# Performance work log

Hardware: AMD Instinct MI355X
Metric: run time of the kernel (lower is better)

## Reference

```python
import jax, jax.numpy as jnp
import numpy as np

B, L, H = 2, 4096, 1024


def _rope_tables(seq_len, dim, base=10000.0):
    # standard RoPE cos/sin tables, rotate-half convention, shape [L, dim]
    inv_freq = 1.0 / (base ** (np.arange(0, dim, 2, dtype=np.float32) / dim))
    t = np.arange(seq_len, dtype=np.float32)
    freqs = np.outer(t, inv_freq)                      # [L, dim/2]
    emb = np.concatenate([freqs, freqs], axis=-1)      # [L, dim]
    return jnp.asarray(np.cos(emb)), jnp.asarray(np.sin(emb))


def setup_inputs() -> dict:
    key = jax.random.key(0)
    k1, k2 = jax.random.split(key)
    hidden_states = jax.random.normal(k1, (B, L, H), dtype=jnp.float32)
    # queries weight: normal with std = initializer_range / sqrt(2*num_layers*hidden)
    std = 0.02 / np.sqrt(2.0 * 24 * H)
    W_q = jax.random.normal(k2, (H, H), dtype=jnp.float32) * std
    cos, sin = _rope_tables(L, H)
    return {"hidden_states": hidden_states, "W_q": W_q, "cos": cos, "sin": sin}


def _rotate_half(x):
    x1, x2 = jnp.split(x, 2, axis=-1)
    return jnp.concatenate([-x2, x1], axis=-1)


def reference(hidden_states, W_q, cos, sin):
    # dropout with p=0.0 (eval) -> identity
    h = hidden_states * cos[None, :, :] + _rotate_half(hidden_states) * sin[None, :, :]  # RoPE, [B,L,H]
    q = jnp.einsum('blh,oh->blo', h, W_q)          # F.linear(h, W_q), [B,L,H]
    pre_attn = jnp.einsum('blh,bmh->blm', q, h)    # Q @ K^T (no softmax), [B,L,L]
    attention = jnp.einsum('blm,bmh->blh', pre_attn, h)  # scores @ V, [B,L,H]
    return attention
```

## Files before the change

### kernel.cpp

```cpp
#include <hip/hip_runtime.h>
#include <hip/hip_bf16.h>
#include <stdint.h>

#define BB 2
#define LL 4096
#define HH 1024
#define GBK 32

typedef __bf16 bf16;
typedef __bf16 bf16x4 __attribute__((ext_vector_type(4)));
typedef __bf16 bf16x8 __attribute__((ext_vector_type(8)));
typedef float  f32x4  __attribute__((ext_vector_type(4)));

__device__ __forceinline__ void async_cp16(const bf16* g, const bf16* l)
{
    typedef const uint32_t __attribute__((address_space(1)))* gp_t;
    typedef uint32_t __attribute__((address_space(3)))* lp_t;
    __builtin_amdgcn_global_load_lds((gp_t)(uintptr_t)g, (lp_t)(uintptr_t)l, 16, 0, 0);
}

__global__ __launch_bounds__(128) void rope_kernel(
    const float* __restrict__ x, const float* __restrict__ cs,
    const float* __restrict__ sn, bf16* __restrict__ h)
{
    const int l = blockIdx.x;
    const int b = blockIdx.y;
    const int i = threadIdx.x * 4;
    const long xb = ((long)b * LL + l) * HH;
    const long cb = (long)l * HH;

    const float4 x1 = *(const float4*)(x + xb + i);
    const float4 x2 = *(const float4*)(x + xb + i + HH / 2);
    const float4 c1 = *(const float4*)(cs + cb + i);
    const float4 c2 = *(const float4*)(cs + cb + i + HH / 2);
    const float4 s1 = *(const float4*)(sn + cb + i);
    const float4 s2 = *(const float4*)(sn + cb + i + HH / 2);

    bf16x4 o1, o2;
    o1[0] = (bf16)(x1.x * c1.x - x2.x * s1.x);
    o1[1] = (bf16)(x1.y * c1.y - x2.y * s1.y);
    o1[2] = (bf16)(x1.z * c1.z - x2.z * s1.z);
    o1[3] = (bf16)(x1.w * c1.w - x2.w * s1.w);
    o2[0] = (bf16)(x2.x * c2.x + x1.x * s2.x);
    o2[1] = (bf16)(x2.y * c2.y + x1.y * s2.y);
    o2[2] = (bf16)(x2.z * c2.z + x1.z * s2.z);
    o2[3] = (bf16)(x2.w * c2.w + x1.w * s2.w);

    *(bf16x4*)(h + xb + i)          = o1;
    *(bf16x4*)(h + xb + i + HH / 2) = o2;
}

__global__ __launch_bounds__(256) void transpose_bf16_64(
    const bf16* __restrict__ in, bf16* __restrict__ out, const int R, const int C)
{
    __shared__ uint32_t lds[64][36];
    const long zoff = (long)blockIdx.z * R * C;
    const int r0 = blockIdx.x * 64;
    const int c0 = blockIdx.y * 64;
    const int t  = threadIdx.x;

    const int c8 = t & 7;
    const int rr = t >> 3;
    const bf16* p0 = in + zoff + (long)(r0 + 2 * rr) * C + c0 + c8 * 8;
    const uint4 ra = *(const uint4*)p0;
    const uint4 rb = *(const uint4*)(p0 + C);
    const uint32_t av[4] = {ra.x, ra.y, ra.z, ra.w};
    const uint32_t bv[4] = {rb.x, rb.y, rb.z, rb.w};
#pragma unroll
    for (int j = 0; j < 4; ++j) {
        const uint32_t alo = av[j] & 0xffffu, ahi = av[j] >> 16;
        const uint32_t blo = bv[j] & 0xffffu, bhi = bv[j] >> 16;
        lds[c8 * 8 + 2 * j    ][rr] = alo | (blo << 16);
        lds[c8 * 8 + 2 * j + 1][rr] = ahi | (bhi << 16);
    }
    __syncthreads();

    const int c = t >> 2;
    const int q = t & 3;
    const uint4 w0 = *(const uint4*)&lds[c][q * 8];
    const uint4 w1 = *(const uint4*)&lds[c][q * 8 + 4];
    bf16* po = out + zoff + (long)(c0 + c) * R + r0 + q * 16;
    *(uint4*)(po)     = w0;
    *(uint4*)(po + 8) = w1;
}

__global__ __launch_bounds__(256) void cast_wq(
    const float* __restrict__ Wq, bf16* __restrict__ Wb)
{
    const long idx = ((long)blockIdx.x * 256 + threadIdx.x) * 4;
    const float4 v = *(const float4*)(Wq + idx);
    bf16x4 o;
    o[0] = (bf16)v.x; o[1] = (bf16)v.y; o[2] = (bf16)v.z; o[3] = (bf16)v.w;
    *(bf16x4*)(Wb + idx) = o;
}

#define GEMM_SHARED()                                                          \
    __shared__ __align__(16) bf16 As_[2][128][32];                             \
    __shared__ __align__(16) bf16 Bs_[2][128][32];

#define GEMM_PREFETCH(KOFF, BUF)                                               \
    do {                                                                       \
        async_cp16(Ag + (KOFF),           &As_[BUF][0][0] + woff0);            \
        async_cp16(Ag + (KOFF) + 64L * K, &As_[BUF][0][0] + woff1);            \
        async_cp16(Bg + (KOFF),           &Bs_[BUF][0][0] + woff0);            \
        async_cp16(Bg + (KOFF) + 64L * K, &Bs_[BUF][0][0] + woff1);            \
    } while (0)

#define GEMM_BODY(M0, N0, KBASE, KEND, DST, DT, LDN)                           \
    {                                                                          \
        const int tid  = threadIdx.x;                                          \
        const int lane = tid & 63;                                             \
        const int wave = tid >> 6;                                             \
        const int wm = (wave & 1) * 64;                                        \
        const int wn = (wave >> 1) * 64;                                       \
        const int fr = lane & 15;                                              \
        const int fq = lane >> 4;                                              \
        const int srow = tid >> 2;                                             \
        const int scol = (tid & 3) * 8;                                        \
        const int woff0 = wave * 512;                                          \
        const int woff1 = 2048 + wave * 512;                                   \
        const bf16* Ag = Ab + (long)((M0) + srow) * K + scol;                  \
        const bf16* Bg = Bb + (long)((N0) + srow) * K + scol;                  \
        const f32x4 vzero = {0.f, 0.f, 0.f, 0.f};                              \
        f32x4 acc[4][4];                                                       \
        _Pragma("unroll") for (int i = 0; i < 4; ++i)                          \
            _Pragma("unroll") for (int j = 0; j < 4; ++j) acc[i][j] = vzero;   \
        GEMM_PREFETCH(KBASE, 0);                                               \
        int buf = 0;                                                           \
        for (int k0 = (KBASE); k0 < (KEND); k0 += GBK, buf ^= 1) {             \
            __syncthreads();                                                   \
            if (k0 + GBK < (KEND)) GEMM_PREFETCH(k0 + GBK, buf ^ 1);           \
            bf16x8 af[4], bfv[4];                                              \
            _Pragma("unroll") for (int i = 0; i < 4; ++i)                      \
                af[i]  = *(const bf16x8*)&As_[buf][wm + i * 16 + fr][fq * 8];  \
            _Pragma("unroll") for (int j = 0; j < 4; ++j)                      \
                bfv[j] = *(const bf16x8*)&Bs_[buf][wn + j * 16 + fr][fq * 8];  \
            _Pragma("unroll") for (int i = 0; i < 4; ++i)                      \
                _Pragma("unroll") for (int j = 0; j < 4; ++j)                  \
                    acc[i][j] = __builtin_amdgcn_mfma_f32_16x16x32_bf16(       \
                        af[i], bfv[j], acc[i][j], 0, 0, 0);                    \
        }                                                                      \
        _Pragma("unroll") for (int i = 0; i < 4; ++i) {                        \
            _Pragma("unroll") for (int r = 0; r < 4; ++r) {                    \
                const int row = (M0) + wm + i * 16 + fq * 4 + r;               \
                _Pragma("unroll") for (int j = 0; j < 4; ++j) {                \
                    const int col = (N0) + wn + j * 16 + fr;                   \
                    (DST)[(long)row * (LDN) + col] = (DT)acc[i][j][r];         \
                }                                                              \
            }                                                                  \
        }                                                                      \
    }

template <typename OUT_T>
__global__ __launch_bounds__(256) void gemm_bt(
    const bf16* __restrict__ A, const bf16* __restrict__ B, OUT_T* __restrict__ C,
    const int M, const int N, const int K,
    const long sA, const long sB, const long sC)
{
    GEMM_SHARED();
    const bf16* Ab = A + blockIdx.z * sA;
    const bf16* Bb = B + blockIdx.z * sB;
    OUT_T*      Cb = C + blockIdx.z * sC;
    const int m0 = blockIdx.x * 128;
    const int n0 = blockIdx.y * 128;
    GEMM_BODY(m0, n0, 0, K, Cb, OUT_T, N);
}

#define E_STAGE_A(KT, PART, BUF)                                               \
  do {                                                                         \
    const int kk0_ = kbase + (KT) * 64;                                        \
    _Pragma("unroll") for (int qq_ = 0; qq_ < 2; ++qq_) {                      \
      const int ch_  = qq_ * 512 + tid;                                        \
      const int sl_  = ch_ >> 3;                                               \
      const int cc_  = (ch_ & 7) ^ (sl_ & 7);                                  \
      const int row_ = (sl_ & 63) + (PART) * 64 + ((sl_ >> 6) << 7);           \
      async_cp16(Ab + (long)(m0 + row_) * K + kk0_ + cc_ * 8,                  \
                 &As[BUF][PART][0][0] + (qq_ * 512 + (tid & 448)) * 8);        \
    }                                                                          \
  } while (0)

#define E_STAGE_B(KT, PART, BUF)                                               \
  do {                                                                         \
    const int kk0_ = kbase + (KT) * 64;                                        \
    _Pragma("unroll") for (int qq_ = 0; qq_ < 2; ++qq_) {                      \
      const int ch_  = qq_ * 512 + tid;                                        \
      const int sl_  = ch_ >> 3;                                               \
      const int cc_  = (ch_ & 7) ^ (sl_ & 7);                                  \
      const int row_ = (sl_ & 31) + (PART) * 32 + ((sl_ >> 5) << 6);           \
      async_cp16(Bb + (long)(n0 + row_) * K + kk0_ + cc_ * 8,                  \
                 &Bs[BUF][PART][0][0] + (qq_ * 512 + (tid & 448)) * 8);        \
    }                                                                          \
  } while (0)

#define E_LOAD_A(BUF, IG)                                                      \
  do {                                                                         \
    const bf16* Ap_ = &As[BUF][IG][0][0] + (wr * 64 + fr) * 64;                \
    _Pragma("unroll") for (int ii_ = 0; ii_ < 4; ++ii_)                        \
      _Pragma("unroll") for (int kk_ = 0; kk_ < 2; ++kk_)                      \
        af[ii_][kk_] = *(const bf16x8*)(Ap_ + ii_ * 1024 +                     \
                        (((kk_ * 4 + fq) ^ fr7) * 8));                         \
  } while (0)

#define E_LOAD_B(BUF, JP)                                                      \
  do {                                                                         \
    const bf16* Bp_ = &Bs[BUF][JP][0][0] + (wc * 32 + fr) * 64;                \
    _Pragma("unroll") for (int jj_ = 0; jj_ < 2; ++jj_)                        \
      _Pragma("unroll") for (int kk_ = 0; kk_ < 2; ++kk_)                      \
        bfv[jj_][kk_] = *(const bf16x8*)(Bp_ + jj_ * 1024 +                    \
                        (((kk_ * 4 + fq) ^ fr7) * 8));                         \
  } while (0)

#define E_MMA(IG, JG)                                                          \
  do {                                                                         \
    __builtin_amdgcn_s_setprio(1);                                             \
    _Pragma("unroll") for (int ii_ = 0; ii_ < 4; ++ii_)                        \
      _Pragma("unroll") for (int jj_ = 0; jj_ < 2; ++jj_)                      \
        _Pragma("unroll") for (int kk_ = 0; kk_ < 2; ++kk_)                    \
          acc[(IG) * 4 + ii_][(JG) * 2 + jj_] =                                \
              __builtin_amdgcn_mfma_f32_16x16x32_bf16(                         \
                  af[ii_][kk_], bfv[jj_][kk_],                                 \
                  acc[(IG) * 4 + ii_][(JG) * 2 + jj_], 0, 0, 0);               \
    __builtin_amdgcn_s_setprio(0);                                             \
  } while (0)

#define E_BAR()   __builtin_amdgcn_s_barrier()
#define E_LGKM0() do { asm volatile("s_waitcnt lgkmcnt(0)" ::: "memory");      \
                       __builtin_amdgcn_sched_barrier(0); } while (0)
#define E_VM(N)   asm volatile("s_waitcnt vmcnt(" #N ")" ::: "memory")

#define ENGINE_PREAMBLE()                                                      \
  __shared__ __align__(16) bf16 As[2][2][128][64];                             \
  __shared__ __align__(16) bf16 Bs[2][2][128][64];                             \
  const int tid  = threadIdx.x;                                                \
  const int lane = tid & 63;                                                   \
  const int wv   = tid >> 6;                                                   \
  const int wr   = wv >> 2;                                                    \
  const int wc   = wv & 3;                                                     \
  const int fr   = lane & 15;                                                  \
  const int fq   = lane >> 4;                                                  \
  const int fr7  = fr & 7;                                                     \
  bf16x8 af[4][2], bfv[2][2];                                                  \
  f32x4 acc[8][4];                                                             \
  _Pragma("unroll") for (int i_ = 0; i_ < 8; ++i_)                             \
    _Pragma("unroll") for (int j_ = 0; j_ < 4; ++j_)                           \
      acc[i_][j_] = (f32x4){0.f, 0.f, 0.f, 0.f};

#define ENGINE_LOOP(NT)                                                        \
    \
  E_STAGE_A(0, 0, 0); E_STAGE_B(0, 1, 0); E_STAGE_A(0, 1, 0);                  \
  E_STAGE_B(0, 0, 0);                                                          \
  E_STAGE_A(1, 0, 1); E_STAGE_B(1, 1, 1); E_STAGE_A(1, 1, 1);                  \
  E_VM(6); E_BAR();                                                            \
  int t_ = 0;                                                                  \
  _Pragma("unroll 1") for (; t_ + 3 < (NT); t_ += 2) {                         \
     E_LOAD_A(0, 0); E_LOAD_B(0, 0); E_STAGE_B(t_ + 1, 0, 1);          \
             E_BAR(); E_LGKM0(); E_MMA(0, 0); E_BAR();                         \
     E_LOAD_B(0, 1); E_STAGE_A(t_ + 2, 0, 0);                          \
             E_BAR(); E_LGKM0(); E_MMA(0, 1); E_BAR();                         \
     E_LOAD_A(0, 1); E_STAGE_B(t_ + 2, 1, 0);                          \
             E_BAR(); E_LGKM0(); E_MMA(1, 1); E_BAR();                         \
     E_LOAD_B(0, 0); E_STAGE_A(t_ + 2, 1, 0);                          \
             E_BAR(); E_LGKM0(); E_MMA(1, 0); E_VM(6); E_BAR();                \
     E_LOAD_A(1, 0); E_LOAD_B(1, 0); E_STAGE_B(t_ + 2, 0, 0);          \
             E_BAR(); E_LGKM0(); E_MMA(0, 0); E_BAR();                         \
     E_LOAD_B(1, 1); E_STAGE_A(t_ + 3, 0, 1);                          \
             E_BAR(); E_LGKM0(); E_MMA(0, 1); E_BAR();                         \
     E_LOAD_A(1, 1); E_STAGE_B(t_ + 3, 1, 1);                          \
             E_BAR(); E_LGKM0(); E_MMA(1, 1); E_BAR();                         \
     E_LOAD_B(1, 0); E_STAGE_A(t_ + 3, 1, 1);                          \
             E_BAR(); E_LGKM0(); E_MMA(1, 0); E_VM(6); E_BAR();                \
  }                                                                            \
                  \
  E_LOAD_A(0, 0); E_LOAD_B(0, 0); E_STAGE_B(t_ + 1, 0, 1);                     \
  E_BAR(); E_LGKM0(); E_MMA(0, 0); E_BAR();                                    \
  E_LOAD_B(0, 1); E_BAR(); E_LGKM0(); E_MMA(0, 1); E_BAR();                    \
  E_LOAD_A(0, 1); E_BAR(); E_LGKM0(); E_MMA(1, 1); E_BAR();                    \
  E_LOAD_B(0, 0); E_BAR(); E_LGKM0(); E_MMA(1, 0); E_VM(0); E_BAR();           \
  E_LOAD_A(1, 0); E_LOAD_B(1, 0); E_BAR(); E_LGKM0(); E_MMA(0, 0); E_BAR();    \
  E_LOAD_B(1, 1); E_BAR(); E_LGKM0(); E_MMA(0, 1); E_BAR();                    \
  E_LOAD_A(1, 1); E_BAR(); E_LGKM0(); E_MMA(1, 1); E_BAR();                    \
  E_LOAD_B(1, 0); E_BAR(); E_LGKM0(); E_MMA(1, 0);

#define ENGINE_STORE(DST, DT, LDN)                                             \
  _Pragma("unroll") for (int gi_ = 0; gi_ < 8; ++gi_) {                        \
    _Pragma("unroll") for (int r_ = 0; r_ < 4; ++r_) {                         \
      const int row_ = m0 + wr * 128 + gi_ * 16 + fq * 4 + r_;                 \
      _Pragma("unroll") for (int gj_ = 0; gj_ < 4; ++gj_) {                    \
        const int col_ = n0 + wc * 64 + gj_ * 16 + fr;                         \
        (DST)[(long)row_ * (LDN) + col_] = (DT)acc[gi_][gj_][r_];              \
      }                                                                        \
    }                                                                          \
  }

__global__ __launch_bounds__(512, 2) void gemm8_Gq(
    const bf16* __restrict__ hT, const bf16* __restrict__ Wb,
    const bf16* __restrict__ h, float* __restrict__ P, bf16* __restrict__ q)
{
    ENGINE_PREAMBLE();
    const int id = blockIdx.x;
    const bf16* Ab; const bf16* Bb;
    int K, kbase, m0, n0;
    float* Pc = nullptr;
    if (id < 128) {
        m0 = (id & 31) * 256;
        n0 = (id >> 5) * 256;
        Ab = h; Bb = Wb; K = HH; kbase = 0;
    } else {
        const int u  = id - 128;
        const int zb = u >> 6;
        const int v  = u & 63;
        const int zs = v >> 4;
        const int tl = v & 15;
        m0 = (tl & 3) * 256;
        n0 = (tl >> 2) * 256;
        Ab = hT + (long)zb * HH * LL; Bb = Ab;
        K  = LL; kbase = zs * (LL / 4);
        Pc = P + (long)(zb * 4 + zs) * HH * HH;
    }
    ENGINE_LOOP(16);
    if (Pc) { ENGINE_STORE(Pc, float, HH); }
    else    { ENGINE_STORE(q,  bf16,  HH); }
}

__global__ __launch_bounds__(512, 2) void gemm8_qG(
    const bf16* __restrict__ q, const bf16* __restrict__ G, float* __restrict__ out)
{
    ENGINE_PREAMBLE();
    const int id = blockIdx.x;
    const int b  = id >> 6;
    const int u  = id & 63;
    const int m0 = (u & 15) * 256;
    const int n0 = (u >> 4) * 256;
    const bf16* Ab = q + (long)b * LL * HH;
    const bf16* Bb = G + (long)b * HH * HH;
    const int K = HH, kbase = 0;
    float* outb = out + (long)b * LL * HH;
    ENGINE_LOOP(16);
    ENGINE_STORE(outb, float, HH);
}

__global__ __launch_bounds__(256) void reduce_splits(
    const float* __restrict__ P, bf16* __restrict__ out, const int npb, const int S)
{
    const int b = blockIdx.y;
    const long r = ((long)blockIdx.x * 256 + threadIdx.x) * 4;
    const float* base = P + (long)b * S * npb + r;
    float4 a = *(const float4*)(base);
    for (int s = 1; s < S; ++s) {
        const float4 v = *(const float4*)(base + (long)s * npb);
        a.x += v.x; a.y += v.y; a.z += v.z; a.w += v.w;
    }
    bf16x4 o;
    o[0] = (bf16)a.x; o[1] = (bf16)a.y; o[2] = (bf16)a.z; o[3] = (bf16)a.w;
    *(bf16x4*)(out + (long)b * npb + r) = o;
}

extern "C" void kernel_launch(void* const* d_in, const int* in_sizes, int n_in,
                              void* d_out, int out_size, void* d_ws, size_t ws_size,
                              hipStream_t stream)
{
    const float* x  = (const float*)d_in[0];
    const float* Wq = (const float*)d_in[1];
    const float* cs = (const float*)d_in[2];
    const float* sn = (const float*)d_in[3];
    float* out = (float*)d_out;
    char* ws = (char*)d_ws;

    bf16*  h  = (bf16*)(ws);
    bf16*  hT = (bf16*)(ws + 16u * 1024 * 1024);
    bf16*  Wb = (bf16*)(ws + 32u * 1024 * 1024);
    bf16*  G  = (bf16*)(ws + 34u * 1024 * 1024);
    float* P  = (float*)(ws + 38u * 1024 * 1024);

    const bool big_ws = ws_size >= (size_t)90 * 1024 * 1024;
    bf16* q = big_ws ? (bf16*)(ws + 70u * 1024 * 1024)
                     : (bf16*)(ws + 38u * 1024 * 1024);

    rope_kernel<<<dim3(LL, BB), 128, 0, stream>>>(x, cs, sn, h);

    transpose_bf16_64<<<dim3(LL / 64, HH / 64, BB), 256, 0, stream>>>(h, hT, LL, HH);

    cast_wq<<<dim3(HH * HH / 1024), 256, 0, stream>>>(Wq, Wb);

    if (big_ws) {
        gemm8_Gq<<<dim3(256), 512, 0, stream>>>(hT, Wb, h, P, q);
        reduce_splits<<<dim3(HH * HH / 1024, BB), 256, 0, stream>>>(P, G, HH * HH, 4);
        gemm8_qG<<<dim3(128), 512, 0, stream>>>(q, G, out);
    } else {
        gemm_bt<bf16><<<dim3(HH / 128, HH / 128, BB), 256, 0, stream>>>(
            hT, hT, G, HH, HH, LL, (long)HH * LL, (long)HH * LL, (long)HH * HH);
        gemm_bt<bf16><<<dim3(LL / 128, HH / 128, BB), 256, 0, stream>>>(
            h, Wb, q, LL, HH, HH, (long)LL * HH, 0L, (long)LL * HH);
        gemm_bt<float><<<dim3(LL / 128, HH / 128, BB), 256, 0, stream>>>(
            q, G, out, LL, HH, HH, (long)LL * HH, (long)HH * HH, (long)LL * HH);
    }
}
```

Before: 190.9 us.

## Fuse RoPE, transpose and weight cast; halve final GEMM tile for more blocks

Replaces the separate RoPE, transpose and W_q cast launches with one prep kernel that computes RoPE, writes h, transposes through LDS into hT, and casts W_q. This drops the re-read of h for the transpose and two launch gaps. The final q·G GEMM moves to 256x128 tiles, giving 256 blocks instead of 128 to fill more CUs on MI355X. The main loop also reuses B fragments across two MMA groups, saving one LDS fragment load per half-step. In exchange, the smaller tiles give less reuse per block and the prep kernel carries more register pressure.

```diff
diff --git a/kernel.cpp b/kernel.cpp
--- a/kernel.cpp
+++ b/kernel.cpp
@@ -17,6 +17,91 @@
     typedef const uint32_t __attribute__((address_space(1)))* gp_t;
     typedef uint32_t __attribute__((address_space(3)))* lp_t;
     __builtin_amdgcn_global_load_lds((gp_t)(uintptr_t)g, (lp_t)(uintptr_t)l, 16, 0, 0);
+}
+
+__device__ __forceinline__ uint32_t pack_bf16(float lo, float hi)
+{
+    union { bf16 b; unsigned short u; } a, c;
+    a.b = (bf16)lo; c.b = (bf16)hi;
+    return (uint32_t)a.u | ((uint32_t)c.u << 16);
+}
+
+__global__ __launch_bounds__(256) void prep_kernel(
+    const float* __restrict__ x, const float* __restrict__ cs,
+    const float* __restrict__ sn, const float* __restrict__ Wq,
+    bf16* __restrict__ h, bf16* __restrict__ hT, bf16* __restrict__ Wb)
+{
+    const int id = blockIdx.x;
+    if (id >= 1024) {
+        const long base = (long)(id - 1024) * 4096 + (long)threadIdx.x * 16;
+#pragma unroll
+        for (int j = 0; j < 4; ++j) {
+            const float4 v = *(const float4*)(Wq + base + j * 4);
+            bf16x4 o;
+            o[0] = (bf16)v.x; o[1] = (bf16)v.y; o[2] = (bf16)v.z; o[3] = (bf16)v.w;
+            *(bf16x4*)(Wb + base + j * 4) = o;
+        }
+        return;
+    }
+    __shared__ uint32_t lds[2][64][36];
+    const int b  = id >> 9;
+    const int v  = id & 511;
+    const int r0 = (v >> 3) * 64;
+    const int c0 = (v & 7) * 64;
+    const int t  = threadIdx.x;
+    const int c8 = t & 7;
+    const int rr = t >> 3;
+    const int ca = c0 + c8 * 8;
+    const long xrow0 = ((long)b * LL + r0 + 2 * rr) * HH;
+    const long crow0 = (long)(r0 + 2 * rr) * HH;
+
+    float oA[2][8], oB[2][8];
+#pragma unroll
+    for (int rw = 0; rw < 2; ++rw) {
+        const long xr = xrow0 + (long)rw * HH;
+        const long cr = crow0 + (long)rw * HH;
+        float xA[8], xB[8], cA[8], cB[8], sA[8], sB[8];
+        *(float4*)&xA[0] = *(const float4*)(x + xr + ca);
+        *(float4*)&xA[4] = *(const float4*)(x + xr + ca + 4);
+        *(float4*)&xB[0] = *(const float4*)(x + xr + ca + 512);
+        *(float4*)&xB[4] = *(const float4*)(x + xr + ca + 516);
+        *(float4*)&cA[0] = *(const float4*)(cs + cr + ca);
+        *(float4*)&cA[4] = *(const float4*)(cs + cr + ca + 4);
+        *(float4*)&cB[0] = *(const float4*)(cs + cr + ca + 512);
+        *(float4*)&cB[4] = *(const float4*)(cs + cr + ca + 516);
+        *(float4*)&sA[0] = *(const float4*)(sn + cr + ca);
+        *(float4*)&sA[4] = *(const float4*)(sn + cr + ca + 4);
+        *(float4*)&sB[0] = *(const float4*)(sn + cr + ca + 512);
+        *(float4*)&sB[4] = *(const float4*)(sn + cr + ca + 516);
+#pragma unroll
+        for (int j = 0; j < 8; ++j) {
+            oA[rw][j] = xA[j] * cA[j] - xB[j] * sA[j];
+            oB[rw][j] = xB[j] * cB[j] + xA[j] * sB[j];
+        }
+        bf16x8 hA, hB;
+#pragma unroll
+        for (int j = 0; j < 8; ++j) { hA[j] = (bf16)oA[rw][j]; hB[j] = (bf16)oB[rw][j]; }
+        *(bf16x8*)(h + xr + ca)       = hA;
+        *(bf16x8*)(h + xr + ca + 512) = hB;
+    }
+#pragma unroll
+    for (int j = 0; j < 8; ++j) {
+        lds[0][c8 * 8 + j][rr] = pack_bf16(oA[0][j], oA[1][j]);
+        lds[1][c8 * 8 + j][rr] = pack_bf16(oB[0][j], oB[1][j]);
+    }
+    __syncthreads();
+
+    const int cc = t >> 2;
+    const int q  = t & 3;
+#pragma unroll
+    for (int s = 0; s < 2; ++s) {
+        const int hrow = (s ? c0 + 512 : c0) + cc;
+        bf16* po = hT + (long)b * HH * LL + (long)hrow * LL + r0 + q * 16;
+        const uint4 w0 = *(const uint4*)&lds[s][cc][q * 8];
+        const uint4 w1 = *(const uint4*)&lds[s][cc][q * 8 + 4];
+        *(uint4*)(po)     = w0;
+        *(uint4*)(po + 8) = w1;
+    }
 }
 
 __global__ __launch_bounds__(128) void rope_kernel(
@@ -28,14 +113,12 @@
     const int i = threadIdx.x * 4;
     const long xb = ((long)b * LL + l) * HH;
     const long cb = (long)l * HH;
-
     const float4 x1 = *(const float4*)(x + xb + i);
     const float4 x2 = *(const float4*)(x + xb + i + HH / 2);
     const float4 c1 = *(const float4*)(cs + cb + i);
     const float4 c2 = *(const float4*)(cs + cb + i + HH / 2);
     const float4 s1 = *(const float4*)(sn + cb + i);
     const float4 s2 = *(const float4*)(sn + cb + i + HH / 2);
-
     bf16x4 o1, o2;
     o1[0] = (bf16)(x1.x * c1.x - x2.x * s1.x);
     o1[1] = (bf16)(x1.y * c1.y - x2.y * s1.y);
@@ -45,7 +128,6 @@
     o2[1] = (bf16)(x2.y * c2.y + x1.y * s2.y);
     o2[2] = (bf16)(x2.z * c2.z + x1.z * s2.z);
     o2[3] = (bf16)(x2.w * c2.w + x1.w * s2.w);
-
     *(bf16x4*)(h + xb + i)          = o1;
     *(bf16x4*)(h + xb + i + HH / 2) = o2;
 }
@@ -58,7 +140,6 @@
     const int r0 = blockIdx.x * 64;
     const int c0 = blockIdx.y * 64;
     const int t  = threadIdx.x;
-
     const int c8 = t & 7;
     const int rr = t >> 3;
     const bf16* p0 = in + zoff + (long)(r0 + 2 * rr) * C + c0 + c8 * 8;
@@ -74,7 +155,6 @@
         lds[c8 * 8 + 2 * j + 1][rr] = ahi | (bhi << 16);
     }
     __syncthreads();
-
     const int c = t >> 2;
     const int q = t & 3;
     const uint4 w0 = *(const uint4*)&lds[c][q * 8];
@@ -192,6 +272,16 @@
     }                                                                          \
   } while (0)
 
+#define E_STAGE_B2(KT, PART, BUF)                                              \
+  do {                                                                         \
+    const int kk0_ = kbase + (KT) * 64;                                        \
+    const int sl_  = tid >> 3;                                                 \
+    const int cc_  = (tid & 7) ^ (sl_ & 7);                                    \
+    const int row_ = (sl_ & 15) + (PART) * 16 + ((sl_ >> 4) << 5);             \
+    async_cp16(Bb + (long)(n0 + row_) * K + kk0_ + cc_ * 8,                    \
+               &Bs2[BUF][PART][0][0] + (tid & 448) * 8);                       \
+  } while (0)
+
 #define E_LOAD_A(BUF, IG)                                                      \
   do {                                                                         \
     const bf16* Ap_ = &As[BUF][IG][0][0] + (wr * 64 + fr) * 64;                \
@@ -201,16 +291,23 @@
                         (((kk_ * 4 + fq) ^ fr7) * 8));                         \
   } while (0)
 
-#define E_LOAD_B(BUF, JP)                                                      \
+#define E_LOAD_Bv(BUF, JP, DSTV)                                               \
   do {                                                                         \
     const bf16* Bp_ = &Bs[BUF][JP][0][0] + (wc * 32 + fr) * 64;                \
     _Pragma("unroll") for (int jj_ = 0; jj_ < 2; ++jj_)                        \
       _Pragma("unroll") for (int kk_ = 0; kk_ < 2; ++kk_)                      \
-        bfv[jj_][kk_] = *(const bf16x8*)(Bp_ + jj_ * 1024 +                    \
+        DSTV[jj_][kk_] = *(const bf16x8*)(Bp_ + jj_ * 1024 +                   \
                         (((kk_ * 4 + fq) ^ fr7) * 8));                         \
   } while (0)
 
-#define E_MMA(IG, JG)                                                          \
+#define E_LOAD_B2(BUF, JG, DSTV)                                               \
+  do {                                                                         \
+    const bf16* Bp_ = &Bs2[BUF][JG][0][0] + (wc * 16 + fr) * 64;               \
+    _Pragma("unroll") for (int kk_ = 0; kk_ < 2; ++kk_)                        \
+      DSTV[kk_] = *(const bf16x8*)(Bp_ + (((kk_ * 4 + fq) ^ fr7) * 8));        \
+  } while (0)
+
+#define E_MMA(IG, JG, BV)                                                      \
   do {                                                                         \
     __builtin_amdgcn_s_setprio(1);                                             \
     _Pragma("unroll") for (int ii_ = 0; ii_ < 4; ++ii_)                        \
@@ -218,8 +315,19 @@
         _Pragma("unroll") for (int kk_ = 0; kk_ < 2; ++kk_)                    \
           acc[(IG) * 4 + ii_][(JG) * 2 + jj_] =                                \
               __builtin_amdgcn_mfma_f32_16x16x32_bf16(                         \
-                  af[ii_][kk_], bfv[jj_][kk_],                                 \
+                  af[ii_][kk_], BV[jj_][kk_],                                  \
                   acc[(IG) * 4 + ii_][(JG) * 2 + jj_], 0, 0, 0);               \
+    __builtin_amdgcn_s_setprio(0);                                             \
+  } while (0)
+
+#define E_MMA2(IG, JG, BV)                                                     \
+  do {                                                                         \
+    __builtin_amdgcn_s_setprio(1);                                             \
+    _Pragma("unroll") for (int ii_ = 0; ii_ < 4; ++ii_)                        \
+      _Pragma("unroll") for (int kk_ = 0; kk_ < 2; ++kk_)                      \
+        acc2[(IG) * 4 + ii_][JG] =                                             \
+            __builtin_amdgcn_mfma_f32_16x16x32_bf16(                           \
+                af[ii_][kk_], BV[kk_], acc2[(IG) * 4 + ii_][JG], 0, 0, 0);     \
     __builtin_amdgcn_s_setprio(0);                                             \
   } while (0)
 
@@ -228,9 +336,7 @@
                        __builtin_amdgcn_sched_barrier(0); } while (0)
 #define E_VM(N)   asm volatile("s_waitcnt vmcnt(" #N ")" ::: "memory")
 
-#define ENGINE_PREAMBLE()                                                      \
-  __shared__ __align__(16) bf16 As[2][2][128][64];                             \
-  __shared__ __align__(16) bf16 Bs[2][2][128][64];                             \
+#define E_COMMON_IDX()                                                         \
   const int tid  = threadIdx.x;                                                \
   const int lane = tid & 63;                                                   \
   const int wv   = tid >> 6;                                                   \
@@ -239,64 +345,22 @@
   const int fr   = lane & 15;                                                  \
   const int fq   = lane >> 4;                                                  \
   const int fr7  = fr & 7;                                                     \
-  bf16x8 af[4][2], bfv[2][2];                                                  \
-  f32x4 acc[8][4];                                                             \
-  _Pragma("unroll") for (int i_ = 0; i_ < 8; ++i_)                             \
-    _Pragma("unroll") for (int j_ = 0; j_ < 4; ++j_)                           \
-      acc[i_][j_] = (f32x4){0.f, 0.f, 0.f, 0.f};
-
-#define ENGINE_LOOP(NT)                                                        \
-    \
-  E_STAGE_A(0, 0, 0); E_STAGE_B(0, 1, 0); E_STAGE_A(0, 1, 0);                  \
-  E_STAGE_B(0, 0, 0);                                                          \
-  E_STAGE_A(1, 0, 1); E_STAGE_B(1, 1, 1); E_STAGE_A(1, 1, 1);                  \
-  E_VM(6); E_BAR();                                                            \
-  int t_ = 0;                                                                  \
-  _Pragma("unroll 1") for (; t_ + 3 < (NT); t_ += 2) {                         \
-     E_LOAD_A(0, 0); E_LOAD_B(0, 0); E_STAGE_B(t_ + 1, 0, 1);          \
-             E_BAR(); E_LGKM0(); E_MMA(0, 0); E_BAR();                         \
-     E_LOAD_B(0, 1); E_STAGE_A(t_ + 2, 0, 0);                          \
-             E_BAR(); E_LGKM0(); E_MMA(0, 1); E_BAR();                         \
-     E_LOAD_A(0, 1); E_STAGE_B(t_ + 2, 1, 0);                          \
-             E_BAR(); E_LGKM0(); E_MMA(1, 1); E_BAR();                         \
-     E_LOAD_B(0, 0); E_STAGE_A(t_ + 2, 1, 0);                          \
-             E_BAR(); E_LGKM0(); E_MMA(1, 0); E_VM(6); E_BAR();                \
-     E_LOAD_A(1, 0); E_LOAD_B(1, 0); E_STAGE_B(t_ + 2, 0, 0);          \
-             E_BAR(); E_LGKM0(); E_MMA(0, 0); E_BAR();                         \
-     E_LOAD_B(1, 1); E_STAGE_A(t_ + 3, 0, 1);                          \
-             E_BAR(); E_LGKM0(); E_MMA(0, 1); E_BAR();                         \
-     E_LOAD_A(1, 1); E_STAGE_B(t_ + 3, 1, 1);                          \
-             E_BAR(); E_LGKM0(); E_MMA(1, 1); E_BAR();                         \
-     E_LOAD_B(1, 0); E_STAGE_A(t_ + 3, 1, 1);                          \
-             E_BAR(); E_LGKM0(); E_MMA(1, 0); E_VM(6); E_BAR();                \
-  }                                                                            \
-                  \
-  E_LOAD_A(0, 0); E_LOAD_B(0, 0); E_STAGE_B(t_ + 1, 0, 1);                     \
-  E_BAR(); E_LGKM0(); E_MMA(0, 0); E_BAR();                                    \
-  E_LOAD_B(0, 1); E_BAR(); E_LGKM0(); E_MMA(0, 1); E_BAR();                    \
-  E_LOAD_A(0, 1); E_BAR(); E_LGKM0(); E_MMA(1, 1); E_BAR();                    \
-  E_LOAD_B(0, 0); E_BAR(); E_LGKM0(); E_MMA(1, 0); E_VM(0); E_BAR();           \
-  E_LOAD_A(1, 0); E_LOAD_B(1, 0); E_BAR(); E_LGKM0(); E_MMA(0, 0); E_BAR();    \
-  E_LOAD_B(1, 1); E_BAR(); E_LGKM0(); E_MMA(0, 1); E_BAR();                    \
-  E_LOAD_A(1, 1); E_BAR(); E_LGKM0(); E_MMA(1, 1); E_BAR();                    \
-  E_LOAD_B(1, 0); E_BAR(); E_LGKM0(); E_MMA(1, 0);
-
-#define ENGINE_STORE(DST, DT, LDN)                                             \
-  _Pragma("unroll") for (int gi_ = 0; gi_ < 8; ++gi_) {                        \
-    _Pragma("unroll") for (int r_ = 0; r_ < 4; ++r_) {                         \
-      const int row_ = m0 + wr * 128 + gi_ * 16 + fq * 4 + r_;                 \
-      _Pragma("unroll") for (int gj_ = 0; gj_ < 4; ++gj_) {                    \
-        const int col_ = n0 + wc * 64 + gj_ * 16 + fr;                         \
-        (DST)[(long)row_ * (LDN) + col_] = (DT)acc[gi_][gj_][r_];              \
-      }                                                                        \
-    }                                                                          \
-  }
+  (void)lane;
 
 __global__ __launch_bounds__(512, 2) void gemm8_Gq(
     const bf16* __restrict__ hT, const bf16* __restrict__ Wb,
     const bf16* __restrict__ h, float* __restrict__ P, bf16* __restrict__ q)
 {
-    ENGINE_PREAMBLE();
+    __shared__ __align__(16) bf16 As[2][2][128][64];
+    __shared__ __align__(16) bf16 Bs[2][2][128][64];
+    E_COMMON_IDX();
+    bf16x8 af[4][2], bfv0[2][2], bfv1[2][2];
+    f32x4 acc[8][4];
+#pragma unroll
+    for (int i_ = 0; i_ < 8; ++i_)
+#pragma unroll
+        for (int j_ = 0; j_ < 4; ++j_) acc[i_][j_] = (f32x4){0.f, 0.f, 0.f, 0.f};
+
     const int id = blockIdx.x;
     const bf16* Ab; const bf16* Bb;
     int K, kbase, m0, n0;
@@ -317,26 +381,130 @@
         K  = LL; kbase = zs * (LL / 4);
         Pc = P + (long)(zb * 4 + zs) * HH * HH;
     }
-    ENGINE_LOOP(16);
-    if (Pc) { ENGINE_STORE(Pc, float, HH); }
-    else    { ENGINE_STORE(q,  bf16,  HH); }
+
+    E_STAGE_A(0, 0, 0); E_STAGE_B(0, 1, 0); E_STAGE_A(0, 1, 0);
+    E_STAGE_B(0, 0, 0);
+    E_STAGE_A(1, 0, 1); E_STAGE_B(1, 1, 1); E_STAGE_A(1, 1, 1);
+    E_VM(6); E_BAR();
+    int t_ = 0;
+#pragma unroll 1
+    for (; t_ + 3 < 16; t_ += 2) {
+         E_LOAD_A(0, 0); E_LOAD_Bv(0, 0, bfv0); E_STAGE_B(t_ + 1, 0, 1);
+                 E_BAR(); E_LGKM0(); E_MMA(0, 0, bfv0); E_BAR();
+         E_LOAD_Bv(0, 1, bfv1); E_STAGE_A(t_ + 2, 0, 0);
+                 E_BAR(); E_LGKM0(); E_MMA(0, 1, bfv1); E_BAR();
+         E_LOAD_A(0, 1); E_STAGE_B(t_ + 2, 1, 0);
+                 E_BAR(); E_LGKM0(); E_MMA(1, 1, bfv1); E_BAR();
+         E_STAGE_A(t_ + 2, 1, 0);
+                 E_MMA(1, 0, bfv0); E_VM(6); E_BAR();
+         E_LOAD_A(1, 0); E_LOAD_Bv(1, 0, bfv0); E_STAGE_B(t_ + 2, 0, 0);
+                 E_BAR(); E_LGKM0(); E_MMA(0, 0, bfv0); E_BAR();
+         E_LOAD_Bv(1, 1, bfv1); E_STAGE_A(t_ + 3, 0, 1);
+                 E_BAR(); E_LGKM0(); E_MMA(0, 1, bfv1); E_BAR();
+         E_LOAD_A(1, 1); E_STAGE_B(t_ + 3, 1, 1);
+                 E_BAR(); E_LGKM0(); E_MMA(1, 1, bfv1); E_BAR();
+         E_STAGE_A(t_ + 3, 1, 1);
+                 E_MMA(1, 0, bfv0); E_VM(6); E_BAR();
+    }
+    E_LOAD_A(0, 0); E_LOAD_Bv(0, 0, bfv0); E_STAGE_B(t_ + 1, 0, 1);
+    E_BAR(); E_LGKM0(); E_MMA(0, 0, bfv0); E_BAR();
+    E_LOAD_Bv(0, 1, bfv1); E_BAR(); E_LGKM0(); E_MMA(0, 1, bfv1); E_BAR();
+    E_LOAD_A(0, 1); E_BAR(); E_LGKM0(); E_MMA(1, 1, bfv1); E_BAR();
+    E_MMA(1, 0, bfv0); E_VM(0); E_BAR();
+    E_LOAD_A(1, 0); E_LOAD_Bv(1, 0, bfv0); E_BAR(); E_LGKM0(); E_MMA(0, 0, bfv0); E_BAR();
+    E_LOAD_Bv(1, 1, bfv1); E_BAR(); E_LGKM0(); E_MMA(0, 1, bfv1); E_BAR();
+    E_LOAD_A(1, 1); E_BAR(); E_LGKM0(); E_MMA(1, 1, bfv1); E_BAR();
+    E_MMA(1, 0, bfv0);
+
+    if (Pc) {
+#pragma unroll
+        for (int gi = 0; gi < 8; ++gi)
+#pragma unroll
+            for (int r = 0; r < 4; ++r) {
+                const int row = m0 + wr * 128 + gi * 16 + fq * 4 + r;
+#pragma unroll
+                for (int gj = 0; gj < 4; ++gj)
+                    Pc[(long)row * HH + n0 + wc * 64 + gj * 16 + fr] = acc[gi][gj][r];
+            }
+    } else {
+#pragma unroll
+        for (int gi = 0; gi < 8; ++gi)
+#pragma unroll
+            for (int r = 0; r < 4; ++r) {
+                const int row = m0 + wr * 128 + gi * 16 + fq * 4 + r;
+#pragma unroll
+                for (int gj = 0; gj < 4; ++gj)
+                    q[(long)row * HH + n0 + wc * 64 + gj * 16 + fr] = (bf16)acc[gi][gj][r];
+            }
+    }
 }
 
 __global__ __launch_bounds__(512, 2) void gemm8_qG(
-    const bf16* __restrict__ q, const bf16* __restrict__ G, float* __restrict__ out)
-{
-    ENGINE_PREAMBLE();
+    const bf16* __restrict__ qm, const bf16* __restrict__ G, float* __restrict__ out)
+{
+    __shared__ __align__(16) bf16 As[2][2][128][64];
+    __shared__ __align__(16) bf16 Bs2[2][2][64][64];
+    E_COMMON_IDX();
+    bf16x8 af[4][2], bw0[2], bw1[2];
+    f32x4 acc2[8][2];
+#pragma unroll
+    for (int i_ = 0; i_ < 8; ++i_)
+#pragma unroll
+        for (int j_ = 0; j_ < 2; ++j_) acc2[i_][j_] = (f32x4){0.f, 0.f, 0.f, 0.f};
+
     const int id = blockIdx.x;
-    const int b  = id >> 6;
-    const int u  = id & 63;
+    const int b  = id >> 7;
+    const int u  = id & 127;
     const int m0 = (u & 15) * 256;
-    const int n0 = (u >> 4) * 256;
-    const bf16* Ab = q + (long)b * LL * HH;
+    const int n0 = (u >> 4) * 128;
+    const bf16* Ab = qm + (long)b * LL * HH;
     const bf16* Bb = G + (long)b * HH * HH;
     const int K = HH, kbase = 0;
     float* outb = out + (long)b * LL * HH;
-    ENGINE_LOOP(16);
-    ENGINE_STORE(outb, float, HH);
+
+    E_STAGE_A(0, 0, 0); E_STAGE_B2(0, 1, 0); E_STAGE_A(0, 1, 0);
+    E_STAGE_B2(0, 0, 0);
+    E_STAGE_A(1, 0, 1); E_STAGE_B2(1, 1, 1); E_STAGE_A(1, 1, 1);
+    E_VM(5); E_BAR();
+    int t_ = 0;
+#pragma unroll 1
+    for (; t_ + 3 < 16; t_ += 2) {
+         E_LOAD_A(0, 0); E_LOAD_B2(0, 0, bw0); E_STAGE_B2(t_ + 1, 0, 1);
+                 E_BAR(); E_LGKM0(); E_MMA2(0, 0, bw0); E_BAR();
+         E_LOAD_B2(0, 1, bw1); E_STAGE_A(t_ + 2, 0, 0);
+                 E_BAR(); E_LGKM0(); E_MMA2(0, 1, bw1); E_BAR();
+         E_LOAD_A(0, 1); E_STAGE_B2(t_ + 2, 1, 0);
+                 E_BAR(); E_LGKM0(); E_MMA2(1, 1, bw1); E_BAR();
+         E_STAGE_A(t_ + 2, 1, 0);
+                 E_MMA2(1, 0, bw0); E_VM(5); E_BAR();
+         E_LOAD_A(1, 0); E_LOAD_B2(1, 0, bw0); E_STAGE_B2(t_ + 2, 0, 0);
+                 E_BAR(); E_LGKM0(); E_MMA2(0, 0, bw0); E_BAR();
+         E_LOAD_B2(1, 1, bw1); E_STAGE_A(t_ + 3, 0, 1);
+                 E_BAR(); E_LGKM0(); E_MMA2(0, 1, bw1); E_BAR();
+         E_LOAD_A(1, 1); E_STAGE_B2(t_ + 3, 1, 1);
+                 E_BAR(); E_LGKM0(); E_MMA2(1, 1, bw1); E_BAR();
+         E_STAGE_A(t_ + 3, 1, 1);
+                 E_MMA2(1, 0, bw0); E_VM(5); E_BAR();
+    }
+    E_LOAD_A(0, 0); E_LOAD_B2(0, 0, bw0); E_STAGE_B2(t_ + 1, 0, 1);
+    E_BAR(); E_LGKM0(); E_MMA2(0, 0, bw0); E_BAR();
+    E_LOAD_B2(0, 1, bw1); E_BAR(); E_LGKM0(); E_MMA2(0, 1, bw1); E_BAR();
+    E_LOAD_A(0, 1); E_BAR(); E_LGKM0(); E_MMA2(1, 1, bw1); E_BAR();
+    E_MMA2(1, 0, bw0); E_VM(0); E_BAR();
+    E_LOAD_A(1, 0); E_LOAD_B2(1, 0, bw0); E_BAR(); E_LGKM0(); E_MMA2(0, 0, bw0); E_BAR();
+    E_LOAD_B2(1, 1, bw1); E_BAR(); E_LGKM0(); E_MMA2(0, 1, bw1); E_BAR();
+    E_LOAD_A(1, 1); E_BAR(); E_LGKM0(); E_MMA2(1, 1, bw1); E_BAR();
+    E_MMA2(1, 0, bw0);
+
+#pragma unroll
+    for (int gi = 0; gi < 8; ++gi)
+#pragma unroll
+        for (int r = 0; r < 4; ++r) {
+            const int row = m0 + wr * 128 + gi * 16 + fq * 4 + r;
+#pragma unroll
+            for (int gj = 0; gj < 2; ++gj)
+                outb[(long)row * HH + n0 + wc * 32 + gj * 16 + fr] = acc2[gi][gj][r];
+        }
 }
 
 __global__ __launch_bounds__(256) void reduce_splits(
@@ -376,17 +544,15 @@
     bf16* q = big_ws ? (bf16*)(ws + 70u * 1024 * 1024)
                      : (bf16*)(ws + 38u * 1024 * 1024);
 
-    rope_kernel<<<dim3(LL, BB), 128, 0, stream>>>(x, cs, sn, h);
-
-    transpose_bf16_64<<<dim3(LL / 64, HH / 64, BB), 256, 0, stream>>>(h, hT, LL, HH);
-
-    cast_wq<<<dim3(HH * HH / 1024), 256, 0, stream>>>(Wq, Wb);
-
     if (big_ws) {
+        prep_kernel<<<dim3(1280), 256, 0, stream>>>(x, cs, sn, Wq, h, hT, Wb);
         gemm8_Gq<<<dim3(256), 512, 0, stream>>>(hT, Wb, h, P, q);
         reduce_splits<<<dim3(HH * HH / 1024, BB), 256, 0, stream>>>(P, G, HH * HH, 4);
-        gemm8_qG<<<dim3(128), 512, 0, stream>>>(q, G, out);
+        gemm8_qG<<<dim3(256), 512, 0, stream>>>(q, G, out);
     } else {
+        rope_kernel<<<dim3(LL, BB), 128, 0, stream>>>(x, cs, sn, h);
+        transpose_bf16_64<<<dim3(LL / 64, HH / 64, BB), 256, 0, stream>>>(h, hT, LL, HH);
+        cast_wq<<<dim3(HH * HH / 1024), 256, 0, stream>>>(Wq, Wb);
         gemm_bt<bf16><<<dim3(HH / 128, HH / 128, BB), 256, 0, stream>>>(
             hT, hT, G, HH, HH, LL, (long)HH * LL, (long)HH * LL, (long)HH * HH);
         gemm_bt<bf16><<<dim3(LL / 128, HH / 128, BB), 256, 0, stream>>>(
```

New measurement: 182.6 us. 4.4% less time.
